# Performance work log

Hardware: AMD Instinct MI355X
Metric: run time of the kernel (lower is better)

## Reference

```python
import jax, jax.numpy as jnp
import numpy as np

B = 64       # batch
D = 768      # embed dim
NH = 12      # heads
HD = 64      # head dim
P = 16       # patch size
IMG = 224
G = IMG // P # 14 patches per side
N = G * G    # 196 patch tokens
T = N + 1    # +CLS
M = 4 * D    # MLP hidden 3072
LE = 9       # early blocks (8 prefix + last_early)
LL = 3       # late ragged blocks
NC = 1000    # classes
TAU = 0.9    # ATS CDF keep threshold
SCALE = 1.0 / np.sqrt(float(HD))


def setup_inputs() -> dict:
    keys = iter(jax.random.split(jax.random.key(0), 48))
    def w(shape):
        return jax.random.normal(next(keys), shape, jnp.float32) * 0.02
    def layer_params(L, prefix, d):
        d[prefix + "ln1_g"] = jnp.ones((L, D)); d[prefix + "ln1_b"] = jnp.zeros((L, D))
        d[prefix + "qkv_w"] = w((L, D, 3 * D)); d[prefix + "qkv_b"] = jnp.zeros((L, 3 * D))
        d[prefix + "proj_w"] = w((L, D, D)); d[prefix + "proj_b"] = jnp.zeros((L, D))
        d[prefix + "ln2_g"] = jnp.ones((L, D)); d[prefix + "ln2_b"] = jnp.zeros((L, D))
        d[prefix + "fc1_w"] = w((L, D, M)); d[prefix + "fc1_b"] = jnp.zeros((L, M))
        d[prefix + "fc2_w"] = w((L, M, D)); d[prefix + "fc2_b"] = jnp.zeros((L, D))
    inp = {}
    inp["images"] = jax.random.normal(next(keys), (B, 3, IMG, IMG), jnp.float32)
    inp["patch_w"] = w((D, 3, P, P)); inp["patch_b"] = jnp.zeros((D,))
    inp["cls_token"] = w((1, 1, D)); inp["pos_embed"] = w((1, T, D))
    layer_params(LE, "e_", inp)
    layer_params(LL, "l_", inp)
    inp["norm_g"] = jnp.ones((D,)); inp["norm_b"] = jnp.zeros((D,))
    inp["head_w"] = w((D, NC)); inp["head_b"] = jnp.zeros((NC,))
    return inp


def _ln(x, g, b):
    m = x.mean(-1, keepdims=True)
    v = ((x - m) ** 2).mean(-1, keepdims=True)
    return (x - m) * jax.lax.rsqrt(v + 1e-6) * g + b


def _block(x, p, i, key_mask=None):
    # Pre-LN ViT block; returns (x, post-softmax attention weights).
    Bb, Tt, _ = x.shape
    y = _ln(x, p["ln1_g"][i], p["ln1_b"][i])
    qkv = (y @ p["qkv_w"][i] + p["qkv_b"][i]).reshape(Bb, Tt, 3, NH, HD)
    q, k, v = jnp.moveaxis(qkv, 2, 0)                      # each [B,T,H,HD]
    logits = jnp.einsum("bqhd,bkhd->bhqk", q, k) * SCALE
    if key_mask is not None:
        # ragged attention: dropped tokens never act as keys (== packed varlen attn)
        logits = jnp.where(key_mask[:, None, None, :], logits, -1e9)
    a = jax.nn.softmax(logits, axis=-1)
    o = jnp.einsum("bhqk,bkhd->bqhd", a, v).reshape(Bb, Tt, D)
    x = x + o @ p["proj_w"][i] + p["proj_b"][i]
    y = _ln(x, p["ln2_g"][i], p["ln2_b"][i])
    y = jax.nn.gelu(y @ p["fc1_w"][i] + p["fc1_b"][i], approximate=False)
    x = x + y @ p["fc2_w"][i] + p["fc2_b"][i]
    return x, a


def reference(images, patch_w, patch_b, cls_token, pos_embed,
              e_ln1_g, e_ln1_b, e_qkv_w, e_qkv_b, e_proj_w, e_proj_b,
              e_ln2_g, e_ln2_b, e_fc1_w, e_fc1_b, e_fc2_w, e_fc2_b,
              l_ln1_g, l_ln1_b, l_qkv_w, l_qkv_b, l_proj_w, l_proj_b,
              l_ln2_g, l_ln2_b, l_fc1_w, l_fc1_b, l_fc2_w, l_fc2_b,
              norm_g, norm_b, head_w, head_b):
    loc = dict(locals())
    e = {k[2:]: v for k, v in loc.items() if k.startswith("e_")}
    l = {k[2:]: v for k, v in loc.items() if k.startswith("l_")}

    # front: patch embed (stride-P conv as einsum) + CLS + pos
    xi = images.reshape(B, 3, G, P, G, P)
    tok = jnp.einsum("bchpwq,dcpq->bhwd", xi, patch_w).reshape(B, N, D) + patch_b
    x = jnp.concatenate([jnp.broadcast_to(cls_token, (B, 1, D)), tok], axis=1) + pos_embed

    # early prefix + last_early (capture attn)
    attn = None
    for i in range(LE):
        x, attn = _block(x, e, i)

    # ATS importance scores: CLS attention (head-avg) * token feature norm, normalized
    cls_attn = attn.mean(axis=1)[:, 0, 1:]                 # [B,N]
    raw = cls_attn * jnp.linalg.norm(x[:, 1:, :], axis=-1)
    s = raw / (raw.sum(-1, keepdims=True) + 1e-12)

    # CDF mask: keep highest-scoring tokens until cumulative importance reaches TAU
    order = jnp.argsort(-s, axis=-1)
    cdf = jnp.cumsum(jnp.take_along_axis(s, order, axis=-1), axis=-1)
    keep_sorted = (cdf <= TAU).at[:, 0].set(True)          # always keep best token
    mask = jnp.zeros((B, N), bool).at[jnp.arange(B)[:, None], order].set(keep_sorted)
    key_mask = jnp.concatenate([jnp.ones((B, 1), bool), mask], axis=1)  # CLS kept

    # ragged late blocks (masked attention == packed variable-length attention)
    for i in range(LL):
        x, _ = _block(x, l, i, key_mask)

    # back: gather CLS (position 0 == cu_seqlens offsets), norm, head
    cls = _ln(x[:, 0, :], norm_g, norm_b)
    return cls @ head_w + head_b
```

## Files before the change

kernel.cpp:

```cpp
#include <hip/hip_runtime.h>
#include <hip/hip_bf16.h>
#include <math.h>

typedef __attribute__((ext_vector_type(8))) short s16x8;
typedef __attribute__((ext_vector_type(4))) short s16x4;
typedef __attribute__((ext_vector_type(4))) float f32x4;

#define MP 12672
#define MREAL 12608
#define PROWS 12544
#define SCALE 0.125f

__device__ __forceinline__ float gelu_exact(float z) {
    return 0.5f * z * (1.f + erff(z * 0.7071067811865475f));
}

__global__ void zero_pad_rows(float* __restrict__ x) {
    int r = MREAL + blockIdx.x;
    x[(size_t)r * 768 + threadIdx.x] = 0.f;
}

__global__ void set_cls(const float* __restrict__ cls, const float* __restrict__ pos,
                        float* __restrict__ x) {
    int b = blockIdx.x, t = threadIdx.x;
    x[(size_t)b * 197 * 768 + t] = cls[t] + pos[t];
}

__global__ void cast_pw(const float* __restrict__ w, __hip_bfloat16* __restrict__ o, int n) {
    int i = blockIdx.x * 256 + threadIdx.x;
    if (i < n) o[i] = __float2bfloat16(w[i]);
}

__global__ void im2col_kernel(const float* __restrict__ img, __hip_bfloat16* __restrict__ P) {
    int row = blockIdx.x;
    int t = threadIdx.x;
    if (row >= PROWS) {
        for (int k = t; k < 768; k += 256) P[(size_t)row * 768 + k] = __float2bfloat16(0.f);
        return;
    }
    int b = row / 196, n = row % 196;
    int gh = n / 14, gw = n % 14;
    for (int k = t; k < 768; k += 256) {
        int c = k >> 8, rem = k & 255, p = rem >> 4, q = rem & 15;
        float v = img[((size_t)(b * 3 + c) * 224 + (gh * 16 + p)) * 224 + gw * 16 + q];
        P[(size_t)row * 768 + k] = __float2bfloat16(v);
    }
}

__global__ void transpose_cast_all(const float* __restrict__ qkvw,
                                   const float* __restrict__ projw,
                                   const float* __restrict__ fc1w,
                                   const float* __restrict__ fc2w,
                                   __hip_bfloat16* __restrict__ wt) {
    __shared__ float tile[32][33];
    int bid = blockIdx.x;
    const float* W; __hip_bfloat16* D; int K, N, tn;
    if (bid < 1728) { W = qkvw; D = wt; K = 768; N = 2304; tn = 72; }
    else if (bid < 2304) { bid -= 1728; W = projw; D = wt + 1769472; K = 768; N = 768; tn = 24; }
    else if (bid < 4608) { bid -= 2304; W = fc1w; D = wt + 2359296; K = 768; N = 3072; tn = 96; }
    else { bid -= 4608; W = fc2w; D = wt + 4718592; K = 3072; N = 768; tn = 24; }
    int n0 = (bid % tn) * 32, k0 = (bid / tn) * 32;
    int tx = threadIdx.x, ty = threadIdx.y;
    #pragma unroll
    for (int i = 0; i < 4; ++i)
        tile[ty + i * 8][tx] = W[(size_t)(k0 + ty + i * 8) * N + n0 + tx];
    __syncthreads();
    #pragma unroll
    for (int i = 0; i < 4; ++i)
        D[(size_t)(n0 + ty + i * 8) * K + k0 + tx] = __float2bfloat16(tile[tx][ty + i * 8]);
}

__global__ void ln_bf16(const float* __restrict__ x, const float* __restrict__ g,
                        const float* __restrict__ bia, __hip_bfloat16* __restrict__ y) {
    int row = blockIdx.x;
    const float* xr = x + (size_t)row * 768;
    __hip_bfloat16* yr = y + (size_t)row * 768;
    int t = threadIdx.x;
    float v[3];
    float s = 0.f, s2 = 0.f;
    #pragma unroll
    for (int i = 0; i < 3; ++i) { v[i] = xr[t + 256 * i]; s += v[i]; s2 += v[i] * v[i]; }
    __shared__ float r1[256], r2[256];
    r1[t] = s; r2[t] = s2; __syncthreads();
    for (int off = 128; off > 0; off >>= 1) {
        if (t < off) { r1[t] += r1[t + off]; r2[t] += r2[t + off]; }
        __syncthreads();
    }
    float mean = r1[0] * (1.f / 768.f);
    float var = r2[0] * (1.f / 768.f) - mean * mean;
    float rs = rsqrtf(var + 1e-6f);
    #pragma unroll
    for (int i = 0; i < 3; ++i) {
        int c = t + 256 * i;
        yr[c] = __float2bfloat16((v[i] - mean) * rs * g[c] + bia[c]);
    }
}

__global__ void ln_cls_t(const float* __restrict__ x, const float* __restrict__ g,
                         const float* __restrict__ bia, float* __restrict__ At) {
    int b = blockIdx.x;
    const float* xr = x + (size_t)b * 197 * 768;
    int t = threadIdx.x;
    float v[3];
    float s = 0.f, s2 = 0.f;
    #pragma unroll
    for (int i = 0; i < 3; ++i) { v[i] = xr[t + 256 * i]; s += v[i]; s2 += v[i] * v[i]; }
    __shared__ float r1[256], r2[256];
    r1[t] = s; r2[t] = s2; __syncthreads();
    for (int off = 128; off > 0; off >>= 1) {
        if (t < off) { r1[t] += r1[t + off]; r2[t] += r2[t + off]; }
        __syncthreads();
    }
    float mean = r1[0] * (1.f / 768.f);
    float var = r2[0] * (1.f / 768.f) - mean * mean;
    float rs = rsqrtf(var + 1e-6f);
    #pragma unroll
    for (int i = 0; i < 3; ++i) {
        int c = t + 256 * i;
        At[(size_t)c * 64 + b] = (v[i] - mean) * rs * g[c] + bia[c];
    }
}

template <int EPI>
__global__ __launch_bounds__(256)
void gemm_mfma(const __hip_bfloat16* __restrict__ A,
               const __hip_bfloat16* __restrict__ Bt,
               const float* __restrict__ bias,
               const float* res, float* Cf, __hip_bfloat16* Cb,
               const float* __restrict__ pos,
               int Nc, int K) {
    __shared__ short As[8192];
    __shared__ short Bs[8192];
    int tid = threadIdx.x;
    int lane = tid & 63, w = tid >> 6;
    int wr = w >> 1, wc = w & 1;
    int nwg = gridDim.x * gridDim.y;
    int bid = blockIdx.y * gridDim.x + blockIdx.x;
    int xcd = bid & 7, idx = bid >> 3;
    int qq = nwg >> 3, rr = nwg & 7;
    int swz = (xcd < rr ? xcd * (qq + 1) : rr * (qq + 1) + (xcd - rr) * qq) + idx;
    int bm = (swz / gridDim.x) * 128, bn = (swz % gridDim.x) * 128;
    int l15 = lane & 15, lh = lane >> 4;
    f32x4 acc[4][4] = {};
    for (int k0 = 0; k0 < K; k0 += 64) {
        #pragma unroll
        for (int q = 0; q < 4; ++q) {
            int S = (w * 4 + q) * 64 + lane;
            int row = S >> 3;
            int c = (S & 7) ^ (row & 7);
            const __hip_bfloat16* sA = A + (size_t)(bm + row) * K + (k0 + c * 8);
            const __hip_bfloat16* sB = Bt + (size_t)(bn + row) * K + (k0 + c * 8);
            __builtin_amdgcn_global_load_lds(
                (const __attribute__((address_space(1))) void*)sA,
                (__attribute__((address_space(3))) void*)&As[(w * 4 + q) * 512], 16, 0, 0);
            __builtin_amdgcn_global_load_lds(
                (const __attribute__((address_space(1))) void*)sB,
                (__attribute__((address_space(3))) void*)&Bs[(w * 4 + q) * 512], 16, 0, 0);
        }
        __syncthreads();
        #pragma unroll
        for (int ks = 0; ks < 2; ++ks) {
            s16x8 av[4], bv[4];
            int c = ks * 4 + lh;
            #pragma unroll
            for (int i = 0; i < 4; ++i) {
                int ra = wr * 64 + i * 16 + l15;
                av[i] = *(const s16x8*)&As[(ra * 8 + (c ^ (ra & 7))) * 8];
                int rb = wc * 64 + i * 16 + l15;
                bv[i] = *(const s16x8*)&Bs[(rb * 8 + (c ^ (rb & 7))) * 8];
            }
            #pragma unroll
            for (int i = 0; i < 4; ++i)
                #pragma unroll
                for (int j = 0; j < 4; ++j)
                    acc[i][j] = __builtin_amdgcn_mfma_f32_16x16x32_bf16(av[i], bv[j], acc[i][j], 0, 0, 0);
        }
        __syncthreads();
    }
    #pragma unroll
    for (int i = 0; i < 4; ++i) {
        #pragma unroll
        for (int j = 0; j < 4; ++j) {
            int colg = bn + wc * 64 + j * 16 + l15;
            float bcol = bias[colg];
            #pragma unroll
            for (int r = 0; r < 4; ++r) {
                int rowg = bm + wr * 64 + i * 16 + lh * 4 + r;
                float v = acc[i][j][r] + bcol;
                if (EPI == 0) {
                    Cf[(size_t)rowg * Nc + colg] = v;
                } else if (EPI == 1) {
                    Cf[(size_t)rowg * Nc + colg] = v + res[(size_t)rowg * Nc + colg];
                } else if (EPI == 2) {
                    Cb[(size_t)rowg * Nc + colg] = __float2bfloat16(gelu_exact(v));
                } else if (EPI == 4) {
                    Cb[(size_t)rowg * Nc + colg] = __float2bfloat16(v);
                } else {
                    if (rowg < PROWS) {
                        int b = rowg / 196, n = rowg % 196;
                        Cf[((size_t)b * 197 + 1 + n) * 768 + colg] = v + pos[(size_t)(1 + n) * 768 + colg];
                    }
                }
            }
        }
    }
}

__global__ __launch_bounds__(256)
void attn_mfma(const __hip_bfloat16* __restrict__ qkvp, const int* __restrict__ key_mask,
               __hip_bfloat16* __restrict__ o, float* __restrict__ cls_row,
               int useMask, int saveCls) {
    int h = blockIdx.x, b = blockIdx.y;
    __shared__ short Kl[224 * 64];
    __shared__ short Vt[64 * 256];
    __shared__ short Pl[4][4096];
    __shared__ unsigned mword[7];
    const short* qkv = (const short*)qkvp;
    int t = threadIdx.x;

    if (t < 7) {
        unsigned wb = 0;
        for (int j = 0; j < 32; ++j) {
            int k = t * 32 + j;
            int bit = (k < 197) ? (useMask ? (key_mask[b * 197 + k] != 0) : 1) : 0;
            wb |= (unsigned)bit << j;
        }
        mword[t] = wb;
    }
    {
        int c = t & 7, kr0 = t >> 3;
        for (int it = 0; it < 7; ++it) {
            int krow = kr0 + it * 32;
            s16x8 v;
            if (krow < 197) {
                v = *(const s16x8*)(qkv + (size_t)(b * 197 + krow) * 2304 + 768 + h * 64 + c * 8);
            } else {
                #pragma unroll
                for (int j = 0; j < 8; ++j) v[j] = 0;
            }
            *(s16x8*)&Kl[(krow * 8 + (c ^ (krow & 7))) * 8] = v;
        }
    }
    {
        int d = t & 63, cb = t >> 6;
        for (int it = 0; it < 8; ++it) {
            int c = cb + it * 4;
            s16x8 v;
            #pragma unroll
            for (int j = 0; j < 8; ++j) {
                int k = c * 8 + j;
                v[j] = (k < 197) ? qkv[(size_t)(b * 197 + k) * 2304 + 1536 + h * 64 + d] : (short)0;
            }
            *(s16x8*)&Vt[(d * 32 + (c ^ (d & 7))) * 8] = v;
        }
    }
    __syncthreads();

    int w = t >> 6, lane = t & 63;
    int l15 = lane & 15, lh = lane >> 4;
    unsigned mw[7];
    #pragma unroll
    for (int i = 0; i < 7; ++i) mw[i] = mword[i];
    short* Pw = &Pl[w][0];

    for (int qf = w; qf < 13; qf += 4) {
        int qbase = qf * 16;
        int q = qbase + l15;
        const short* qptr = qkv + (size_t)(b * 197 + q) * 2304 + h * 64;
        s16x8 bq0 = *(const s16x8*)(qptr + lh * 8);
        s16x8 bq1 = *(const s16x8*)(qptr + 32 + lh * 8);

        f32x4 sacc[14];
        #pragma unroll
        for (int mf = 0; mf < 14; ++mf) sacc[mf] = (f32x4){0.f, 0.f, 0.f, 0.f};
        #pragma unroll
        for (int mf = 0; mf < 14; ++mf) {
            int row = mf * 16 + l15;
            s16x8 a0 = *(const s16x8*)&Kl[(row * 8 + (lh ^ (row & 7))) * 8];
            s16x8 a1 = *(const s16x8*)&Kl[(row * 8 + ((4 + lh) ^ (row & 7))) * 8];
            sacc[mf] = __builtin_amdgcn_mfma_f32_16x16x32_bf16(a0, bq0, sacc[mf], 0, 0, 0);
            sacc[mf] = __builtin_amdgcn_mfma_f32_16x16x32_bf16(a1, bq1, sacc[mf], 0, 0, 0);
        }
        float m = -1e30f;
        #pragma unroll
        for (int mf = 0; mf < 14; ++mf) {
            #pragma unroll
            for (int r = 0; r < 4; ++r) {
                int k = mf * 16 + lh * 4 + r;
                int keep = (mw[k >> 5] >> (k & 31)) & 1;
                float lg = keep ? sacc[mf][r] * SCALE : -1e30f;
                sacc[mf][r] = lg;
                m = fmaxf(m, lg);
            }
        }
        m = fmaxf(m, __shfl_xor(m, 16));
        m = fmaxf(m, __shfl_xor(m, 32));
        float sum = 0.f;
        #pragma unroll
        for (int mf = 0; mf < 14; ++mf) {
            #pragma unroll
            for (int r = 0; r < 4; ++r) {
                float p = expf(sacc[mf][r] - m);
                sum += p;
                sacc[mf][r] = p;
            }
        }
        sum += __shfl_xor(sum, 16);
        sum += __shfl_xor(sum, 32);
        float inv = 1.f / sum;
        if (saveCls && qf == 0 && l15 == 0) {
            #pragma unroll
            for (int mf = 0; mf < 14; ++mf)
                #pragma unroll
                for (int r = 0; r < 4; ++r) {
                    int k = mf * 16 + lh * 4 + r;
                    if (k < 197) cls_row[((size_t)b * 12 + h) * 197 + k] = sacc[mf][r] * inv;
                }
        }
        #pragma unroll
        for (int mf = 0; mf < 14; ++mf) {
            s16x4 pk;
            #pragma unroll
            for (int r = 0; r < 4; ++r) {
                __hip_bfloat16 hb = __float2bfloat16(sacc[mf][r] * inv);
                pk[r] = *(short*)&hb;
            }
            int slot = l15 * 32 + ((mf * 2 + (lh >> 1)) ^ (l15 & 7));
            *(s16x4*)&Pw[slot * 8 + (lh & 1) * 4] = pk;
        }
        f32x4 oacc[4];
        #pragma unroll
        for (int nf = 0; nf < 4; ++nf) oacc[nf] = (f32x4){0.f, 0.f, 0.f, 0.f};
        #pragma unroll
        for (int ks = 0; ks < 7; ++ks) {
            int c = ks * 4 + lh;
            s16x8 pa = *(const s16x8*)&Pw[(l15 * 32 + (c ^ (l15 & 7))) * 8];
            #pragma unroll
            for (int nf = 0; nf < 4; ++nf) {
                int d = nf * 16 + l15;
                s16x8 bv = *(const s16x8*)&Vt[(d * 32 + (c ^ (d & 7))) * 8];
                oacc[nf] = __builtin_amdgcn_mfma_f32_16x16x32_bf16(pa, bv, oacc[nf], 0, 0, 0);
            }
        }
        #pragma unroll
        for (int nf = 0; nf < 4; ++nf) {
            #pragma unroll
            for (int r = 0; r < 4; ++r) {
                int q2 = qbase + lh * 4 + r;
                if (q2 < 197)
                    o[(size_t)(b * 197 + q2) * 768 + h * 64 + nf * 16 + l15] =
                        __float2bfloat16(oacc[nf][r]);
            }
        }
    }
}

__global__ void cls_scores(const float* __restrict__ x, const float* __restrict__ cls_row,
                           float* __restrict__ raw) {
    int bn = blockIdx.x;
    int b = bn / 196, n = bn % 196;
    const float* xr = x + ((size_t)b * 197 + 1 + n) * 768;
    int t = threadIdx.x;
    float s2 = 0.f;
    for (int c = t; c < 768; c += 256) { float v = xr[c]; s2 += v * v; }
    __shared__ float r[256];
    r[t] = s2; __syncthreads();
    for (int off = 128; off > 0; off >>= 1) {
        if (t < off) r[t] += r[t + off];
        __syncthreads();
    }
    if (t == 0) {
        float ca = 0.f;
        for (int h = 0; h < 12; ++h) ca += cls_row[((size_t)b * 12 + h) * 197 + 1 + n];
        raw[bn] = (ca * (1.f / 12.f)) * sqrtf(r[0]);
    }
}

__global__ void ats_mask_kernel(const float* __restrict__ raw, int* __restrict__ key_mask) {
    int b = blockIdx.x, t = threadIdx.x;
    __shared__ float s[196];
    __shared__ float ssorted[196];
    __shared__ int keep[196];
    __shared__ float red[256];
    float v = (t < 196) ? raw[b * 196 + t] : 0.f;
    red[t] = v; __syncthreads();
    for (int off = 128; off > 0; off >>= 1) {
        if (t < off) red[t] += red[t + off];
        __syncthreads();
    }
    float total = red[0];
    if (t < 196) s[t] = v / (total + 1e-12f);
    __syncthreads();
    int rk = 0;
    if (t < 196) {
        float mys = s[t];
        for (int j = 0; j < 196; ++j) {
            float sj = s[j];
            rk += (sj > mys) || (sj == mys && j < t);
        }
        ssorted[rk] = mys;
    }
    __syncthreads();
    if (t == 0) {
        float c = 0.f;
        for (int k = 0; k < 196; ++k) {
            c += ssorted[k];
            keep[k] = (c <= 0.9f) || (k == 0);
        }
    }
    __syncthreads();
    if (t == 0) key_mask[b * 197] = 1;
    if (t < 196) key_mask[b * 197 + 1 + t] = keep[rk];
}

__global__ void gemm_head_t(const float* __restrict__ At, const float* __restrict__ W,
                            const float* __restrict__ bias, float* __restrict__ out) {
    int col = blockIdx.x;
    int t = threadIdx.x;
    int row = t & 63, part = t >> 6;
    float acc = 0.f;
    for (int i = 0; i < 192; ++i) {
        int k = part * 192 + i;
        acc += At[(size_t)k * 64 + row] * W[(size_t)k * 1000 + col];
    }
    __shared__ float red[256];
    red[t] = acc; __syncthreads();
    if (part == 0)
        out[(size_t)row * 1000 + col] = red[row] + red[64 + row] + red[128 + row] + red[192 + row]
                                        + bias[col];
}

extern "C" void kernel_launch(void* const* d_in, const int* in_sizes, int n_in,
                              void* d_out, int out_size, void* d_ws, size_t ws_size,
                              hipStream_t stream) {
    const float* images  = (const float*)d_in[0];
    const float* patch_w = (const float*)d_in[1];
    const float* patch_b = (const float*)d_in[2];
    const float* cls_tok = (const float*)d_in[3];
    const float* pos_emb = (const float*)d_in[4];
    const float* e_p[12]; const float* l_p[12];
    for (int i = 0; i < 12; ++i) e_p[i] = (const float*)d_in[5 + i];
    for (int i = 0; i < 12; ++i) l_p[i] = (const float*)d_in[17 + i];
    const float* norm_g = (const float*)d_in[29];
    const float* norm_b = (const float*)d_in[30];
    const float* head_w = (const float*)d_in[31];
    const float* head_b = (const float*)d_in[32];
    float* out = (float*)d_out;

    float* ws = (float*)d_ws;
    size_t off = 0;
    float* x = ws + off; off += (size_t)MP * 768;
    __hip_bfloat16* ybf = (__hip_bfloat16*)(ws + off); off += (size_t)MP * 768 / 2;
    float* qh = ws + off; off += (size_t)MP * 3072;
    __hip_bfloat16* qbf = (__hip_bfloat16*)qh;
    __hip_bfloat16* P = (__hip_bfloat16*)qh;
    __hip_bfloat16* hbf = (__hip_bfloat16*)qh;
    __hip_bfloat16* wt = (__hip_bfloat16*)(ws + off); off += (size_t)7077888 / 2;
    __hip_bfloat16* pwb = (__hip_bfloat16*)(ws + off); off += (size_t)589824 / 2;
    float* clsrow = ws + off; off += (size_t)64 * 12 * 197;
    float* raw = ws + off; off += (size_t)64 * 196;
    float* At = ws + off; off += (size_t)768 * 64;
    int* kmask = (int*)(ws + off); off += (size_t)64 * 197;

    __hip_bfloat16* wt_qkv  = wt;
    __hip_bfloat16* wt_proj = wt_qkv + (size_t)2304 * 768;
    __hip_bfloat16* wt_fc1  = wt_proj + (size_t)768 * 768;
    __hip_bfloat16* wt_fc2  = wt_fc1 + (size_t)3072 * 768;

    zero_pad_rows<<<64, 768, 0, stream>>>(x);
    set_cls<<<64, 768, 0, stream>>>(cls_tok, pos_emb, x);
    cast_pw<<<2304, 256, 0, stream>>>(patch_w, pwb, 589824);
    im2col_kernel<<<MP, 256, 0, stream>>>(images, P);
    gemm_mfma<3><<<dim3(6, 99), 256, 0, stream>>>(P, pwb, patch_b, nullptr, x, nullptr,
                                                  pos_emb, 768, 768);

    for (int blk = 0; blk < 12; ++blk) {
        bool early = blk < 9;
        int i = early ? blk : blk - 9;
        const float* const* p = early ? e_p : l_p;
        const float* ln1g = p[0] + (size_t)i * 768;
        const float* ln1b = p[1] + (size_t)i * 768;
        const float* qkvw = p[2] + (size_t)i * 768 * 2304;
        const float* qkvb = p[3] + (size_t)i * 2304;
        const float* projw = p[4] + (size_t)i * 768 * 768;
        const float* projb = p[5] + (size_t)i * 768;
        const float* ln2g = p[6] + (size_t)i * 768;
        const float* ln2b = p[7] + (size_t)i * 768;
        const float* fc1w = p[8] + (size_t)i * 768 * 3072;
        const float* fc1b = p[9] + (size_t)i * 3072;
        const float* fc2w = p[10] + (size_t)i * 3072 * 768;
        const float* fc2b = p[11] + (size_t)i * 768;
        int useMask = early ? 0 : 1;
        int saveCls = (early && i == 8) ? 1 : 0;

        transpose_cast_all<<<6912, dim3(32, 8), 0, stream>>>(qkvw, projw, fc1w, fc2w, wt);

        ln_bf16<<<MP, 256, 0, stream>>>(x, ln1g, ln1b, ybf);
        gemm_mfma<4><<<dim3(18, 99), 256, 0, stream>>>(ybf, wt_qkv, qkvb, nullptr, nullptr, qbf,
                                                       nullptr, 2304, 768);
        attn_mfma<<<dim3(12, 64), 256, 0, stream>>>(qbf, kmask, ybf, clsrow, useMask, saveCls);
        gemm_mfma<1><<<dim3(6, 99), 256, 0, stream>>>(ybf, wt_proj, projb, x, x, nullptr,
                                                      nullptr, 768, 768);
        ln_bf16<<<MP, 256, 0, stream>>>(x, ln2g, ln2b, ybf);
        gemm_mfma<2><<<dim3(24, 99), 256, 0, stream>>>(ybf, wt_fc1, fc1b, nullptr, nullptr, hbf,
                                                       nullptr, 3072, 768);
        gemm_mfma<1><<<dim3(6, 99), 256, 0, stream>>>(hbf, wt_fc2, fc2b, x, x, nullptr,
                                                      nullptr, 768, 3072);

        if (saveCls) {
            cls_scores<<<12544, 256, 0, stream>>>(x, clsrow, raw);
            ats_mask_kernel<<<64, 256, 0, stream>>>(raw, kmask);
        }
    }

    ln_cls_t<<<64, 256, 0, stream>>>(x, norm_g, norm_b, At);
    gemm_head_t<<<1000, 256, 0, stream>>>(At, head_w, head_b, out);
}
```

Before: 4.894 ms.

## Triple-buffer GEMM with 256-row tiles, wave-per-row layernorm, MFMA priority in attention

The GEMM now uses 512-thread blocks with 256x128 tiles and a three-slot LDS ring. Loads for tile t+2 are issued while tile t is computed, using vmcnt waits and a single barrier per step in place of two syncthreads. Layernorm switches to one wavefront per row with float4 loads and shuffle reductions, removing the shared-memory tree. The attention MFMA loops get s_setprio hints. Padded rows grow to 12800 to fit the taller tiles, which adds some wasted rows and more LDS per block.

```diff
diff --git a/kernel.cpp b/kernel.cpp
--- a/kernel.cpp
+++ b/kernel.cpp
@@ -6,7 +6,7 @@
 typedef __attribute__((ext_vector_type(4))) short s16x4;
 typedef __attribute__((ext_vector_type(4))) float f32x4;
 
-#define MP 12672
+#define MP2 12800
 #define MREAL 12608
 #define PROWS 12544
 #define SCALE 0.125f
@@ -70,29 +70,36 @@
         D[(size_t)(n0 + ty + i * 8) * K + k0 + tx] = __float2bfloat16(tile[tx][ty + i * 8]);
 }
 
-__global__ void ln_bf16(const float* __restrict__ x, const float* __restrict__ g,
-                        const float* __restrict__ bia, __hip_bfloat16* __restrict__ y) {
-    int row = blockIdx.x;
+__global__ void ln_bf16_w(const float* __restrict__ x, const float* __restrict__ g,
+                          const float* __restrict__ bia, __hip_bfloat16* __restrict__ y) {
+    int row = blockIdx.x * 4 + (threadIdx.x >> 6);
+    int lane = threadIdx.x & 63;
     const float* xr = x + (size_t)row * 768;
-    __hip_bfloat16* yr = y + (size_t)row * 768;
-    int t = threadIdx.x;
-    float v[3];
+    f32x4 v[3];
     float s = 0.f, s2 = 0.f;
     #pragma unroll
-    for (int i = 0; i < 3; ++i) { v[i] = xr[t + 256 * i]; s += v[i]; s2 += v[i] * v[i]; }
-    __shared__ float r1[256], r2[256];
-    r1[t] = s; r2[t] = s2; __syncthreads();
-    for (int off = 128; off > 0; off >>= 1) {
-        if (t < off) { r1[t] += r1[t + off]; r2[t] += r2[t + off]; }
-        __syncthreads();
-    }
-    float mean = r1[0] * (1.f / 768.f);
-    float var = r2[0] * (1.f / 768.f) - mean * mean;
+    for (int i = 0; i < 3; ++i) {
+        v[i] = *(const f32x4*)&xr[lane * 4 + i * 256];
+        #pragma unroll
+        for (int j = 0; j < 4; ++j) { s += v[i][j]; s2 += v[i][j] * v[i][j]; }
+    }
+    #pragma unroll
+    for (int off = 1; off < 64; off <<= 1) { s += __shfl_xor(s, off); s2 += __shfl_xor(s2, off); }
+    float mean = s * (1.f / 768.f);
+    float var = s2 * (1.f / 768.f) - mean * mean;
     float rs = rsqrtf(var + 1e-6f);
     #pragma unroll
     for (int i = 0; i < 3; ++i) {
-        int c = t + 256 * i;
-        yr[c] = __float2bfloat16((v[i] - mean) * rs * g[c] + bia[c]);
+        int c = lane * 4 + i * 256;
+        f32x4 gg = *(const f32x4*)&g[c];
+        f32x4 bb = *(const f32x4*)&bia[c];
+        s16x4 o;
+        #pragma unroll
+        for (int j = 0; j < 4; ++j) {
+            __hip_bfloat16 hb = __float2bfloat16((v[i][j] - mean) * rs * gg[j] + bb[j]);
+            o[j] = *(short*)&hb;
+        }
+        *(s16x4*)&y[(size_t)row * 768 + c] = o;
     }
 }
 
@@ -122,15 +129,15 @@
 }
 
 template <int EPI>
-__global__ __launch_bounds__(256)
-void gemm_mfma(const __hip_bfloat16* __restrict__ A,
-               const __hip_bfloat16* __restrict__ Bt,
-               const float* __restrict__ bias,
-               const float* res, float* Cf, __hip_bfloat16* Cb,
-               const float* __restrict__ pos,
-               int Nc, int K) {
-    __shared__ short As[8192];
-    __shared__ short Bs[8192];
+__global__ __launch_bounds__(512, 2)
+void gemm_mfma2(const __hip_bfloat16* __restrict__ A,
+                const __hip_bfloat16* __restrict__ Bt,
+                const float* __restrict__ bias,
+                const float* res, float* Cf, __hip_bfloat16* Cb,
+                const float* __restrict__ pos,
+                int Nc, int K) {
+    __shared__ short As[3 * 16384];
+    __shared__ short Bs[3 * 8192];
     int tid = threadIdx.x;
     int lane = tid & 63, w = tid >> 6;
     int wr = w >> 1, wc = w & 1;
@@ -139,25 +146,40 @@
     int xcd = bid & 7, idx = bid >> 3;
     int qq = nwg >> 3, rr = nwg & 7;
     int swz = (xcd < rr ? xcd * (qq + 1) : rr * (qq + 1) + (xcd - rr) * qq) + idx;
-    int bm = (swz / gridDim.x) * 128, bn = (swz % gridDim.x) * 128;
+    int bm = (swz / gridDim.x) * 256, bn = (swz % gridDim.x) * 128;
     int l15 = lane & 15, lh = lane >> 4;
+    int NT = K >> 6;
+
+    auto STAGE = [&](int t) {
+        int slot = t % 3;
+        #pragma unroll
+        for (int q2 = 0; q2 < 4; ++q2) {
+            int S = q2 * 512 + tid;
+            int row = S >> 3, c = (S & 7) ^ (row & 7);
+            __builtin_amdgcn_global_load_lds(
+                (const __attribute__((address_space(1))) void*)(A + (size_t)(bm + row) * K + t * 64 + c * 8),
+                (__attribute__((address_space(3))) void*)&As[slot * 16384 + S * 8], 16, 0, 0);
+        }
+        #pragma unroll
+        for (int q2 = 0; q2 < 2; ++q2) {
+            int S = q2 * 512 + tid;
+            int row = S >> 3, c = (S & 7) ^ (row & 7);
+            __builtin_amdgcn_global_load_lds(
+                (const __attribute__((address_space(1))) void*)(Bt + (size_t)(bn + row) * K + t * 64 + c * 8),
+                (__attribute__((address_space(3))) void*)&Bs[slot * 8192 + S * 8], 16, 0, 0);
+        }
+    };
+
     f32x4 acc[4][4] = {};
-    for (int k0 = 0; k0 < K; k0 += 64) {
-        #pragma unroll
-        for (int q = 0; q < 4; ++q) {
-            int S = (w * 4 + q) * 64 + lane;
-            int row = S >> 3;
-            int c = (S & 7) ^ (row & 7);
-            const __hip_bfloat16* sA = A + (size_t)(bm + row) * K + (k0 + c * 8);
-            const __hip_bfloat16* sB = Bt + (size_t)(bn + row) * K + (k0 + c * 8);
-            __builtin_amdgcn_global_load_lds(
-                (const __attribute__((address_space(1))) void*)sA,
-                (__attribute__((address_space(3))) void*)&As[(w * 4 + q) * 512], 16, 0, 0);
-            __builtin_amdgcn_global_load_lds(
-                (const __attribute__((address_space(1))) void*)sB,
-                (__attribute__((address_space(3))) void*)&Bs[(w * 4 + q) * 512], 16, 0, 0);
-        }
-        __syncthreads();
+    STAGE(0); STAGE(1);
+    for (int t = 0; t < NT; ++t) {
+        if (t < NT - 1) { asm volatile("s_waitcnt vmcnt(6)" ::: "memory"); }
+        else            { asm volatile("s_waitcnt vmcnt(0)" ::: "memory"); }
+        __builtin_amdgcn_s_barrier();
+        __builtin_amdgcn_sched_barrier(0);
+        if (t + 2 < NT) STAGE(t + 2);
+        const short* Ab = &As[(t % 3) * 16384];
+        const short* Bb = &Bs[(t % 3) * 8192];
         #pragma unroll
         for (int ks = 0; ks < 2; ++ks) {
             s16x8 av[4], bv[4];
@@ -165,9 +187,9 @@
             #pragma unroll
             for (int i = 0; i < 4; ++i) {
                 int ra = wr * 64 + i * 16 + l15;
-                av[i] = *(const s16x8*)&As[(ra * 8 + (c ^ (ra & 7))) * 8];
+                av[i] = *(const s16x8*)&Ab[(ra * 8 + (c ^ (ra & 7))) * 8];
                 int rb = wc * 64 + i * 16 + l15;
-                bv[i] = *(const s16x8*)&Bs[(rb * 8 + (c ^ (rb & 7))) * 8];
+                bv[i] = *(const s16x8*)&Bb[(rb * 8 + (c ^ (rb & 7))) * 8];
             }
             #pragma unroll
             for (int i = 0; i < 4; ++i)
@@ -175,7 +197,6 @@
                 for (int j = 0; j < 4; ++j)
                     acc[i][j] = __builtin_amdgcn_mfma_f32_16x16x32_bf16(av[i], bv[j], acc[i][j], 0, 0, 0);
         }
-        __syncthreads();
     }
     #pragma unroll
     for (int i = 0; i < 4; ++i) {
@@ -273,6 +294,7 @@
         f32x4 sacc[14];
         #pragma unroll
         for (int mf = 0; mf < 14; ++mf) sacc[mf] = (f32x4){0.f, 0.f, 0.f, 0.f};
+        __builtin_amdgcn_s_setprio(1);
         #pragma unroll
         for (int mf = 0; mf < 14; ++mf) {
             int row = mf * 16 + l15;
@@ -281,6 +303,7 @@
             sacc[mf] = __builtin_amdgcn_mfma_f32_16x16x32_bf16(a0, bq0, sacc[mf], 0, 0, 0);
             sacc[mf] = __builtin_amdgcn_mfma_f32_16x16x32_bf16(a1, bq1, sacc[mf], 0, 0, 0);
         }
+        __builtin_amdgcn_s_setprio(0);
         float m = -1e30f;
         #pragma unroll
         for (int mf = 0; mf < 14; ++mf) {
@@ -331,6 +354,7 @@
         f32x4 oacc[4];
         #pragma unroll
         for (int nf = 0; nf < 4; ++nf) oacc[nf] = (f32x4){0.f, 0.f, 0.f, 0.f};
+        __builtin_amdgcn_s_setprio(1);
         #pragma unroll
         for (int ks = 0; ks < 7; ++ks) {
             int c = ks * 4 + lh;
@@ -342,6 +366,7 @@
                 oacc[nf] = __builtin_amdgcn_mfma_f32_16x16x32_bf16(pa, bv, oacc[nf], 0, 0, 0);
             }
         }
+        __builtin_amdgcn_s_setprio(0);
         #pragma unroll
         for (int nf = 0; nf < 4; ++nf) {
             #pragma unroll
@@ -449,9 +474,9 @@
 
     float* ws = (float*)d_ws;
     size_t off = 0;
-    float* x = ws + off; off += (size_t)MP * 768;
-    __hip_bfloat16* ybf = (__hip_bfloat16*)(ws + off); off += (size_t)MP * 768 / 2;
-    float* qh = ws + off; off += (size_t)MP * 3072;
+    float* x = ws + off; off += (size_t)MP2 * 768;
+    __hip_bfloat16* ybf = (__hip_bfloat16*)(ws + off); off += (size_t)MP2 * 768 / 2;
+    float* qh = ws + off; off += (size_t)MP2 * 3072;
     __hip_bfloat16* qbf = (__hip_bfloat16*)qh;
     __hip_bfloat16* P = (__hip_bfloat16*)qh;
     __hip_bfloat16* hbf = (__hip_bfloat16*)qh;
@@ -467,12 +492,12 @@
     __hip_bfloat16* wt_fc1  = wt_proj + (size_t)768 * 768;
     __hip_bfloat16* wt_fc2  = wt_fc1 + (size_t)3072 * 768;
 
-    zero_pad_rows<<<64, 768, 0, stream>>>(x);
+    zero_pad_rows<<<192, 768, 0, stream>>>(x);
     set_cls<<<64, 768, 0, stream>>>(cls_tok, pos_emb, x);
     cast_pw<<<2304, 256, 0, stream>>>(patch_w, pwb, 589824);
-    im2col_kernel<<<MP, 256, 0, stream>>>(images, P);
-    gemm_mfma<3><<<dim3(6, 99), 256, 0, stream>>>(P, pwb, patch_b, nullptr, x, nullptr,
-                                                  pos_emb, 768, 768);
+    im2col_kernel<<<MP2, 256, 0, stream>>>(images, P);
+    gemm_mfma2<3><<<dim3(6, 50), 512, 0, stream>>>(P, pwb, patch_b, nullptr, x, nullptr,
+                                                   pos_emb, 768, 768);
 
     for (int blk = 0; blk < 12; ++blk) {
         bool early = blk < 9;
@@ -495,17 +520,17 @@
 
         transpose_cast_all<<<6912, dim3(32, 8), 0, stream>>>(qkvw, projw, fc1w, fc2w, wt);
 
-        ln_bf16<<<MP, 256, 0, stream>>>(x, ln1g, ln1b, ybf);
-        gemm_mfma<4><<<dim3(18, 99), 256, 0, stream>>>(ybf, wt_qkv, qkvb, nullptr, nullptr, qbf,
-                                                       nullptr, 2304, 768);
+        ln_bf16_w<<<MP2 / 4, 256, 0, stream>>>(x, ln1g, ln1b, ybf);
+        gemm_mfma2<4><<<dim3(18, 50), 512, 0, stream>>>(ybf, wt_qkv, qkvb, nullptr, nullptr, qbf,
+                                                        nullptr, 2304, 768);
         attn_mfma<<<dim3(12, 64), 256, 0, stream>>>(qbf, kmask, ybf, clsrow, useMask, saveCls);
-        gemm_mfma<1><<<dim3(6, 99), 256, 0, stream>>>(ybf, wt_proj, projb, x, x, nullptr,
-                                                      nullptr, 768, 768);
-        ln_bf16<<<MP, 256, 0, stream>>>(x, ln2g, ln2b, ybf);
-        gemm_mfma<2><<<dim3(24, 99), 256, 0, stream>>>(ybf, wt_fc1, fc1b, nullptr, nullptr, hbf,
-                                                       nullptr, 3072, 768);
-        gemm_mfma<1><<<dim3(6, 99), 256, 0, stream>>>(hbf, wt_fc2, fc2b, x, x, nullptr,
-                                                      nullptr, 768, 3072);
+        gemm_mfma2<1><<<dim3(6, 50), 512, 0, stream>>>(ybf, wt_proj, projb, x, x, nullptr,
+                                                       nullptr, 768, 768);
+        ln_bf16_w<<<MP2 / 4, 256, 0, stream>>>(x, ln2g, ln2b, ybf);
+        gemm_mfma2<2><<<dim3(24, 50), 512, 0, stream>>>(ybf, wt_fc1, fc1b, nullptr, nullptr, hbf,
+                                                        nullptr, 3072, 768);
+        gemm_mfma2<1><<<dim3(6, 50), 512, 0, stream>>>(hbf, wt_fc2, fc2b, x, x, nullptr,
+                                                       nullptr, 768, 3072);
 
         if (saveCls) {
             cls_scores<<<12544, 256, 0, stream>>>(x, clsrow, raw);
```

New measurement: 6.433 ms. 31.4% more time.

## Use warp-per-row LayerNorm, hoist GEMM load pointers, raise MFMA priority in attention

Applied to the files above, without the earlier changes.

Replaces the block-per-row LayerNorm, which reduced through shared memory with repeated barriers, with a wavefront-per-row version that does float4 loads and bf16x4 stores and reduces with xor shuffles. Each block now handles four rows. The GEMM precomputes the per-lane global source pointers once and advances them by a constant each k-step, removing the address arithmetic from the inner loop. The attention kernel wraps its MFMA sections in s_setprio to favour matrix-issue waves. The pointer hoisting costs extra live registers, and the priority hints may not help scheduling.

```diff
diff --git a/kernel.cpp b/kernel.cpp
--- a/kernel.cpp
+++ b/kernel.cpp
@@ -70,29 +70,36 @@
         D[(size_t)(n0 + ty + i * 8) * K + k0 + tx] = __float2bfloat16(tile[tx][ty + i * 8]);
 }
 
-__global__ void ln_bf16(const float* __restrict__ x, const float* __restrict__ g,
-                        const float* __restrict__ bia, __hip_bfloat16* __restrict__ y) {
-    int row = blockIdx.x;
+__global__ void ln_bf16_w(const float* __restrict__ x, const float* __restrict__ g,
+                          const float* __restrict__ bia, __hip_bfloat16* __restrict__ y) {
+    int row = blockIdx.x * 4 + (threadIdx.x >> 6);
+    int lane = threadIdx.x & 63;
     const float* xr = x + (size_t)row * 768;
-    __hip_bfloat16* yr = y + (size_t)row * 768;
-    int t = threadIdx.x;
-    float v[3];
+    f32x4 v[3];
     float s = 0.f, s2 = 0.f;
     #pragma unroll
-    for (int i = 0; i < 3; ++i) { v[i] = xr[t + 256 * i]; s += v[i]; s2 += v[i] * v[i]; }
-    __shared__ float r1[256], r2[256];
-    r1[t] = s; r2[t] = s2; __syncthreads();
-    for (int off = 128; off > 0; off >>= 1) {
-        if (t < off) { r1[t] += r1[t + off]; r2[t] += r2[t + off]; }
-        __syncthreads();
-    }
-    float mean = r1[0] * (1.f / 768.f);
-    float var = r2[0] * (1.f / 768.f) - mean * mean;
+    for (int i = 0; i < 3; ++i) {
+        v[i] = *(const f32x4*)&xr[lane * 4 + i * 256];
+        #pragma unroll
+        for (int j = 0; j < 4; ++j) { s += v[i][j]; s2 += v[i][j] * v[i][j]; }
+    }
+    #pragma unroll
+    for (int off = 1; off < 64; off <<= 1) { s += __shfl_xor(s, off); s2 += __shfl_xor(s2, off); }
+    float mean = s * (1.f / 768.f);
+    float var = s2 * (1.f / 768.f) - mean * mean;
     float rs = rsqrtf(var + 1e-6f);
     #pragma unroll
     for (int i = 0; i < 3; ++i) {
-        int c = t + 256 * i;
-        yr[c] = __float2bfloat16((v[i] - mean) * rs * g[c] + bia[c]);
+        int c = lane * 4 + i * 256;
+        f32x4 gg = *(const f32x4*)&g[c];
+        f32x4 bb = *(const f32x4*)&bia[c];
+        s16x4 o;
+        #pragma unroll
+        for (int j = 0; j < 4; ++j) {
+            __hip_bfloat16 hb = __float2bfloat16((v[i][j] - mean) * rs * gg[j] + bb[j]);
+            o[j] = *(short*)&hb;
+        }
+        *(s16x4*)&y[(size_t)row * 768 + c] = o;
     }
 }
 
@@ -141,21 +148,28 @@
     int swz = (xcd < rr ? xcd * (qq + 1) : rr * (qq + 1) + (xcd - rr) * qq) + idx;
     int bm = (swz / gridDim.x) * 128, bn = (swz % gridDim.x) * 128;
     int l15 = lane & 15, lh = lane >> 4;
+    const __hip_bfloat16* pA[4];
+    const __hip_bfloat16* pB[4];
+    #pragma unroll
+    for (int q = 0; q < 4; ++q) {
+        int S = (w * 4 + q) * 64 + lane;
+        int row = S >> 3;
+        int c = (S & 7) ^ (row & 7);
+        pA[q] = A + (size_t)(bm + row) * K + c * 8;
+        pB[q] = Bt + (size_t)(bn + row) * K + c * 8;
+    }
     f32x4 acc[4][4] = {};
     for (int k0 = 0; k0 < K; k0 += 64) {
         #pragma unroll
         for (int q = 0; q < 4; ++q) {
-            int S = (w * 4 + q) * 64 + lane;
-            int row = S >> 3;
-            int c = (S & 7) ^ (row & 7);
-            const __hip_bfloat16* sA = A + (size_t)(bm + row) * K + (k0 + c * 8);
-            const __hip_bfloat16* sB = Bt + (size_t)(bn + row) * K + (k0 + c * 8);
             __builtin_amdgcn_global_load_lds(
-                (const __attribute__((address_space(1))) void*)sA,
+                (const __attribute__((address_space(1))) void*)pA[q],
                 (__attribute__((address_space(3))) void*)&As[(w * 4 + q) * 512], 16, 0, 0);
             __builtin_amdgcn_global_load_lds(
-                (const __attribute__((address_space(1))) void*)sB,
+                (const __attribute__((address_space(1))) void*)pB[q],
                 (__attribute__((address_space(3))) void*)&Bs[(w * 4 + q) * 512], 16, 0, 0);
+            pA[q] += 64;
+            pB[q] += 64;
         }
         __syncthreads();
         #pragma unroll
@@ -273,6 +287,7 @@
         f32x4 sacc[14];
         #pragma unroll
         for (int mf = 0; mf < 14; ++mf) sacc[mf] = (f32x4){0.f, 0.f, 0.f, 0.f};
+        __builtin_amdgcn_s_setprio(1);
         #pragma unroll
         for (int mf = 0; mf < 14; ++mf) {
             int row = mf * 16 + l15;
@@ -281,6 +296,7 @@
             sacc[mf] = __builtin_amdgcn_mfma_f32_16x16x32_bf16(a0, bq0, sacc[mf], 0, 0, 0);
             sacc[mf] = __builtin_amdgcn_mfma_f32_16x16x32_bf16(a1, bq1, sacc[mf], 0, 0, 0);
         }
+        __builtin_amdgcn_s_setprio(0);
         float m = -1e30f;
         #pragma unroll
         for (int mf = 0; mf < 14; ++mf) {
@@ -331,6 +347,7 @@
         f32x4 oacc[4];
         #pragma unroll
         for (int nf = 0; nf < 4; ++nf) oacc[nf] = (f32x4){0.f, 0.f, 0.f, 0.f};
+        __builtin_amdgcn_s_setprio(1);
         #pragma unroll
         for (int ks = 0; ks < 7; ++ks) {
             int c = ks * 4 + lh;
@@ -342,6 +359,7 @@
                 oacc[nf] = __builtin_amdgcn_mfma_f32_16x16x32_bf16(pa, bv, oacc[nf], 0, 0, 0);
             }
         }
+        __builtin_amdgcn_s_setprio(0);
         #pragma unroll
         for (int nf = 0; nf < 4; ++nf) {
             #pragma unroll
@@ -495,13 +513,13 @@
 
         transpose_cast_all<<<6912, dim3(32, 8), 0, stream>>>(qkvw, projw, fc1w, fc2w, wt);
 
-        ln_bf16<<<MP, 256, 0, stream>>>(x, ln1g, ln1b, ybf);
+        ln_bf16_w<<<MP / 4, 256, 0, stream>>>(x, ln1g, ln1b, ybf);
         gemm_mfma<4><<<dim3(18, 99), 256, 0, stream>>>(ybf, wt_qkv, qkvb, nullptr, nullptr, qbf,
                                                        nullptr, 2304, 768);
         attn_mfma<<<dim3(12, 64), 256, 0, stream>>>(qbf, kmask, ybf, clsrow, useMask, saveCls);
         gemm_mfma<1><<<dim3(6, 99), 256, 0, stream>>>(ybf, wt_proj, projb, x, x, nullptr,
                                                       nullptr, 768, 768);
-        ln_bf16<<<MP, 256, 0, stream>>>(x, ln2g, ln2b, ybf);
+        ln_bf16_w<<<MP / 4, 256, 0, stream>>>(x, ln2g, ln2b, ybf);
         gemm_mfma<2><<<dim3(24, 99), 256, 0, stream>>>(ybf, wt_fc1, fc1b, nullptr, nullptr, hbf,
                                                        nullptr, 3072, 768);
         gemm_mfma<1><<<dim3(6, 99), 256, 0, stream>>>(hbf, wt_fc2, fc2b, x, x, nullptr,
```

Result: slower. 5.751 ms (+17.5%).
